# Optimization experiments

Measured on AMD Instinct MI355X. Metric: run time of the kernel, lower is better.

## Reference

```python
import jax, jax.numpy as jnp
import numpy as np

NUM_EMBEDDINGS = 512
EMBEDDING_DIM = 64
COMMITMENT_COST = 0.25


def setup_inputs() -> dict:
    key = jax.random.key(0)
    k1, k2 = jax.random.split(key)
    x = jax.random.normal(k1, (32, 64, 64, 64), dtype=jnp.float32)  # [B, C=D, H, W]
    # torch init: uniform(-1/K, 1/K)
    w = jax.random.uniform(k2, (NUM_EMBEDDINGS, EMBEDDING_DIM), dtype=jnp.float32,
                           minval=-1.0 / NUM_EMBEDDINGS, maxval=1.0 / NUM_EMBEDDINGS)
    return {"x": x, "w": w}


def reference(x, w):
    # [B, C, H, W] -> [B, H, W, C]
    xt = jnp.transpose(x, (0, 2, 3, 1))
    flat = xt.reshape(-1, EMBEDDING_DIM)  # [N, D]
    # squared L2 distances to each codebook vector: [N, K]
    distances = (jnp.sum(flat * flat, axis=1, keepdims=True)
                 + jnp.sum(w * w, axis=1)
                 - 2.0 * flat @ w.T)
    idx = jnp.argmin(distances, axis=1)  # [N]
    encodings = jax.nn.one_hot(idx, NUM_EMBEDDINGS, dtype=x.dtype)  # [N, K]
    quantized = w[idx].reshape(xt.shape)  # gather == one_hot @ w
    e_latent_loss = jnp.mean((jax.lax.stop_gradient(quantized) - xt) ** 2)
    q_latent_loss = jnp.mean((quantized - jax.lax.stop_gradient(xt)) ** 2)
    quant_loss = q_latent_loss + COMMITMENT_COST * e_latent_loss
    # straight-through estimator
    quantized_st = xt + jax.lax.stop_gradient(quantized - xt)
    quantized_out = jnp.transpose(quantized_st, (0, 3, 1, 2))  # back to [B, C, H, W]
    avg_probs = jnp.mean(encodings, axis=0)
    perplexity = jnp.exp(-jnp.sum(avg_probs * jnp.log(avg_probs + 1e-10)))
    return quantized_out, quant_loss, encodings, perplexity
```

## Files before the change

### kernel.cpp

```cpp
#include <hip/hip_runtime.h>
#include <math.h>

#define TB        256
#define POSB      64
#define GROUPS    4
#define KPG       128
#define NPOS      131072
#define KCODES    512
#define DIM       64
#define HW        4096
#define LOSS_OFF  8388608ull
#define ENC_OFF   8388609ull
#define PERP_OFF  75497473ull

__device__ __forceinline__ float tree8(float r0, float r1, float r2, float r3,
                                       float r4, float r5, float r6, float r7) {
    return __fadd_rn(__fadd_rn(__fadd_rn(r0, r1), __fadd_rn(r2, r3)),
                     __fadd_rn(__fadd_rn(r4, r5), __fadd_rn(r6, r7)));
}

extern "C" __global__ __launch_bounds__(512)
void vq_prep(const float* __restrict__ w, float* __restrict__ ww,
             int* __restrict__ counts, float* __restrict__ lossAcc)
{
    const int k = threadIdx.x;
    const float* wk = w + k * DIM;
    float r[8];
    #pragma unroll
    for (int i = 0; i < 8; ++i) {
        #pragma unroll
        for (int j = 0; j < 8; ++j) {
            float v = wk[i * 8 + j];
            float pp = __fmul_rn(v, v);
            r[j] = (i == 0) ? pp : __fadd_rn(r[j], pp);
        }
    }
    ww[k] = tree8(r[0], r[1], r[2], r[3], r[4], r[5], r[6], r[7]);
    counts[k] = 0;
    if (k == 0) *lossAcc = 0.0f;
}

extern "C" __global__ __launch_bounds__(TB)
__attribute__((amdgpu_waves_per_eu(2, 4)))
void vq_main(const float* __restrict__ x, const float* __restrict__ w,
             const float* __restrict__ ww, float* __restrict__ out,
             int* __restrict__ counts, float* __restrict__ lossAcc)
{
    __shared__ float cdist[GROUPS][POSB];
    __shared__ int   ckidx[GROUPS][POSB];
    __shared__ int   hcount[KCODES];

    const int tid = threadIdx.x;
    const int l   = tid & 63;
    const int g   = __builtin_amdgcn_readfirstlane(tid >> 6);
    const int n   = blockIdx.x * POSB + l;
    const int b   = n >> 12;
    const int hw  = n & 4095;

    hcount[tid]      = 0;
    hcount[tid + TB] = 0;

    const float* xp = x + ((size_t)b * DIM) * HW + hw;
    float x2[DIM];
    float r[8];
    #pragma unroll
    for (int i = 0; i < 8; ++i) {
        #pragma unroll
        for (int j = 0; j < 8; ++j) {
            const int d = i * 8 + j;
            float v = xp[(size_t)d * HW];
            x2[d] = v + v;
            float pp = __fmul_rn(v, v);
            r[j] = (i == 0) ? pp : __fadd_rn(r[j], pp);
        }
    }
    const float A = tree8(r[0], r[1], r[2], r[3], r[4], r[5], r[6], r[7]);

    float best  = INFINITY;
    int   bestk = 0;
    const size_t T0 = ENC_OFF + (size_t)blockIdx.x * (POSB * KCODES);
    float4* zs4 = reinterpret_cast<float4*>(out + T0 + 3);
    const float4 zero4 = make_float4(0.0f, 0.0f, 0.0f, 0.0f);

    for (int kk = 0; kk < KPG; ++kk) {
        const int k = g * KPG + kk;
        const float* wk = w + (size_t)k * DIM;
        float s[8];
        #pragma unroll
        for (int i = 0; i < 8; ++i) {
            #pragma unroll
            for (int j = 0; j < 8; ++j) {
                const int d = i * 8 + j;
                if (i == 0) s[j] = __fmul_rn(x2[d], wk[d]);
                else        s[j] = __fmaf_rn(x2[d], wk[d], s[j]);
            }
        }
        float dot  = tree8(s[0], s[1], s[2], s[3], s[4], s[5], s[6], s[7]);
        float t    = __fadd_rn(A, ww[k]);
        float dist = __fadd_rn(t, -dot);
        if (dist < best) { best = dist; bestk = k; }

        if ((kk & 3) == 0) {
            const int m = (kk >> 2) * TB + tid;
            if (m < 8191) zs4[m] = zero4;
        }
    }
    cdist[g][l] = best;
    ckidx[g][l] = bestk;

    if (tid < 3)  out[T0 + tid]   = 0.0f;
    if (tid == 3) out[T0 + 32767] = 0.0f;

    __syncthreads();

    float fb = cdist[0][l];
    int   fk = ckidx[0][l];
    #pragma unroll
    for (int gg = 1; gg < GROUPS; ++gg) {
        float dg = cdist[gg][l];
        int   kg = ckidx[gg][l];
        if (dg < fb) { fb = dg; fk = kg; }
    }

    if (g == 0) {
        out[ENC_OFF + (size_t)n * KCODES + fk] = 1.0f;
        atomicAdd(&hcount[fk], 1);

        const float4* wrow = reinterpret_cast<const float4*>(w + (size_t)fk * DIM);
        float* qo = out + ((size_t)b * DIM) * HW + hw;
        float sse = 0.0f;
        #pragma unroll
        for (int c = 0; c < 16; ++c) {
            float4 q = wrow[c];
            qo[(size_t)(4 * c + 0) * HW] = q.x;
            qo[(size_t)(4 * c + 1) * HW] = q.y;
            qo[(size_t)(4 * c + 2) * HW] = q.z;
            qo[(size_t)(4 * c + 3) * HW] = q.w;
            float e0 = q.x - 0.5f * x2[4 * c + 0]; sse = __fmaf_rn(e0, e0, sse);
            float e1 = q.y - 0.5f * x2[4 * c + 1]; sse = __fmaf_rn(e1, e1, sse);
            float e2 = q.z - 0.5f * x2[4 * c + 2]; sse = __fmaf_rn(e2, e2, sse);
            float e3 = q.w - 0.5f * x2[4 * c + 3]; sse = __fmaf_rn(e3, e3, sse);
        }
        #pragma unroll
        for (int off = 32; off > 0; off >>= 1) sse += __shfl_down(sse, off);
        if (l == 0) atomicAdd(lossAcc, sse);
    }

    __syncthreads();

    {
        int c0 = hcount[tid];       if (c0) atomicAdd(&counts[tid], c0);
        int c1 = hcount[tid + TB];  if (c1) atomicAdd(&counts[tid + TB], c1);
    }
}

extern "C" __global__ __launch_bounds__(512)
void vq_finalize(const int* __restrict__ counts, const float* __restrict__ lossAcc,
                 float* __restrict__ out)
{
    __shared__ double sred[KCODES];
    const int t = threadIdx.x;
    double p = (double)counts[t] * (1.0 / (double)NPOS);
    sred[t] = -p * log(p + 1e-10);
    __syncthreads();
    for (int s = KCODES / 2; s > 0; s >>= 1) {
        if (t < s) sred[t] += sred[t + s];
        __syncthreads();
    }
    if (t == 0) {
        out[PERP_OFF] = (float)exp(sred[0]);
        out[LOSS_OFF] = 1.25f * (lossAcc[0] / 8388608.0f);
    }
}

extern "C" void kernel_launch(void* const* d_in, const int* in_sizes, int n_in,
                              void* d_out, int out_size, void* d_ws, size_t ws_size,
                              hipStream_t stream)
{
    const float* x = (const float*)d_in[0];
    const float* w = (const float*)d_in[1];
    float* out = (float*)d_out;

    float* ww      = (float*)d_ws;
    int*   counts  = (int*)((char*)d_ws + 2048);
    float* lossAcc = (float*)((char*)d_ws + 4096);

    vq_prep<<<1, 512, 0, stream>>>(w, ww, counts, lossAcc);
    vq_main<<<NPOS / POSB, TB, 0, stream>>>(x, w, ww, out, counts, lossAcc);
    vq_finalize<<<1, 512, 0, stream>>>(counts, lossAcc, out);
}
```

Before: 447.1 us.

## Process two positions per thread to reuse codebook loads across positions

Each thread now handles two spatial positions (128 per block), so every codebook weight load feeds two FMAs, halving the weight-load traffic per distance computed. The grid shrinks by half, and the epilogue is split across two wavefronts, one for each position set. The per-thread register footprint roughly doubles (two 64-float x vectors), and waves_per_eu is pinned to 2 to allow that, which lowers occupancy.

```diff
diff --git a/kernel.cpp b/kernel.cpp
--- a/kernel.cpp
+++ b/kernel.cpp
@@ -2,7 +2,7 @@
 #include <math.h>
 
 #define TB        256
-#define POSB      64
+#define POSB      128
 #define GROUPS    4
 #define KPG       128
 #define NPOS      131072
@@ -12,6 +12,8 @@
 #define LOSS_OFF  8388608ull
 #define ENC_OFF   8388609ull
 #define PERP_OFF  75497473ull
+#define TILE_DW   (POSB * KCODES)
+#define NF4       ((TILE_DW - 4) / 4)
 
 __device__ __forceinline__ float tree8(float r0, float r1, float r2, float r3,
                                        float r4, float r5, float r6, float r7) {
@@ -40,8 +42,40 @@
     if (k == 0) *lossAcc = 0.0f;
 }
 
+#define EPILOGUE(X2, P)  do {                                                   \
+    const int p_ = (P);                                                         \
+    float fb = cdist[0][p_];                                                    \
+    int   fk = ckidx[0][p_];                                                    \
+    _Pragma("unroll")                                                           \
+    for (int gg = 1; gg < GROUPS; ++gg) {                                       \
+        float dg = cdist[gg][p_];                                               \
+        int   kg = ckidx[gg][p_];                                               \
+        if (dg < fb) { fb = dg; fk = kg; }                                      \
+    }                                                                           \
+    out[ENC_OFF + (size_t)(blockIdx.x * POSB + p_) * KCODES + fk] = 1.0f;       \
+    atomicAdd(&hcount[fk], 1);                                                  \
+    const float4* wrow = reinterpret_cast<const float4*>(w + (size_t)fk * DIM); \
+    float* qo = out + ((size_t)b * DIM) * HW + (hwb + p_);                      \
+    float sse = 0.0f;                                                           \
+    _Pragma("unroll")                                                           \
+    for (int c = 0; c < 16; ++c) {                                              \
+        float4 q = wrow[c];                                                     \
+        qo[(size_t)(4 * c + 0) * HW] = q.x;                                     \
+        qo[(size_t)(4 * c + 1) * HW] = q.y;                                     \
+        qo[(size_t)(4 * c + 2) * HW] = q.z;                                     \
+        qo[(size_t)(4 * c + 3) * HW] = q.w;                                     \
+        float e0 = q.x - 0.5f * X2[4 * c + 0]; sse = __fmaf_rn(e0, e0, sse);    \
+        float e1 = q.y - 0.5f * X2[4 * c + 1]; sse = __fmaf_rn(e1, e1, sse);    \
+        float e2 = q.z - 0.5f * X2[4 * c + 2]; sse = __fmaf_rn(e2, e2, sse);    \
+        float e3 = q.w - 0.5f * X2[4 * c + 3]; sse = __fmaf_rn(e3, e3, sse);    \
+    }                                                                           \
+    _Pragma("unroll")                                                           \
+    for (int off = 32; off > 0; off >>= 1) sse += __shfl_down(sse, off);        \
+    if (l == 0) atomicAdd(lossAcc, sse);                                        \
+} while (0)
+
 extern "C" __global__ __launch_bounds__(TB)
-__attribute__((amdgpu_waves_per_eu(2, 4)))
+__attribute__((amdgpu_waves_per_eu(2, 2)))
 void vq_main(const float* __restrict__ x, const float* __restrict__ w,
              const float* __restrict__ ww, float* __restrict__ out,
              int* __restrict__ counts, float* __restrict__ lossAcc)
@@ -53,98 +87,88 @@
     const int tid = threadIdx.x;
     const int l   = tid & 63;
     const int g   = __builtin_amdgcn_readfirstlane(tid >> 6);
-    const int n   = blockIdx.x * POSB + l;
-    const int b   = n >> 12;
-    const int hw  = n & 4095;
+    const int hwb = (blockIdx.x * POSB) & 4095;
+    const int b   = (blockIdx.x * POSB) >> 12;
 
     hcount[tid]      = 0;
     hcount[tid + TB] = 0;
 
-    const float* xp = x + ((size_t)b * DIM) * HW + hw;
-    float x2[DIM];
-    float r[8];
-    #pragma unroll
-    for (int i = 0; i < 8; ++i) {
-        #pragma unroll
-        for (int j = 0; j < 8; ++j) {
-            const int d = i * 8 + j;
-            float v = xp[(size_t)d * HW];
-            x2[d] = v + v;
-            float pp = __fmul_rn(v, v);
-            r[j] = (i == 0) ? pp : __fadd_rn(r[j], pp);
-        }
-    }
-    const float A = tree8(r[0], r[1], r[2], r[3], r[4], r[5], r[6], r[7]);
-
-    float best  = INFINITY;
-    int   bestk = 0;
-    const size_t T0 = ENC_OFF + (size_t)blockIdx.x * (POSB * KCODES);
-    float4* zs4 = reinterpret_cast<float4*>(out + T0 + 3);
-    const float4 zero4 = make_float4(0.0f, 0.0f, 0.0f, 0.0f);
-
-    for (int kk = 0; kk < KPG; ++kk) {
-        const int k = g * KPG + kk;
-        const float* wk = w + (size_t)k * DIM;
-        float s[8];
+    const float* xp = x + ((size_t)b * DIM) * HW + (hwb + l);
+    float x2a[DIM], x2b[DIM];
+    float A0, A1;
+    {
+        float ra[8], rb[8];
         #pragma unroll
         for (int i = 0; i < 8; ++i) {
             #pragma unroll
             for (int j = 0; j < 8; ++j) {
                 const int d = i * 8 + j;
-                if (i == 0) s[j] = __fmul_rn(x2[d], wk[d]);
-                else        s[j] = __fmaf_rn(x2[d], wk[d], s[j]);
+                float va = xp[(size_t)d * HW];
+                float vb = xp[(size_t)d * HW + 64];
+                x2a[d] = va + va;
+                x2b[d] = vb + vb;
+                float pa = __fmul_rn(va, va);
+                float pb = __fmul_rn(vb, vb);
+                ra[j] = (i == 0) ? pa : __fadd_rn(ra[j], pa);
+                rb[j] = (i == 0) ? pb : __fadd_rn(rb[j], pb);
             }
         }
-        float dot  = tree8(s[0], s[1], s[2], s[3], s[4], s[5], s[6], s[7]);
-        float t    = __fadd_rn(A, ww[k]);
-        float dist = __fadd_rn(t, -dot);
-        if (dist < best) { best = dist; bestk = k; }
-
-        if ((kk & 3) == 0) {
-            const int m = (kk >> 2) * TB + tid;
-            if (m < 8191) zs4[m] = zero4;
-        }
-    }
-    cdist[g][l] = best;
-    ckidx[g][l] = bestk;
-
-    if (tid < 3)  out[T0 + tid]   = 0.0f;
-    if (tid == 3) out[T0 + 32767] = 0.0f;
+        A0 = tree8(ra[0], ra[1], ra[2], ra[3], ra[4], ra[5], ra[6], ra[7]);
+        A1 = tree8(rb[0], rb[1], rb[2], rb[3], rb[4], rb[5], rb[6], rb[7]);
+    }
+
+    float best0 = INFINITY, best1 = INFINITY;
+    int   bk0 = 0, bk1 = 0;
+    const size_t T0 = ENC_OFF + (size_t)blockIdx.x * TILE_DW;
+    float4* zs4 = reinterpret_cast<float4*>(out + T0 + 3);
+    const float4 zero4 = make_float4(0.0f, 0.0f, 0.0f, 0.0f);
+
+    for (int kk = 0; kk < KPG; ++kk) {
+        const int k = g * KPG + kk;
+        const float* wk = w + (size_t)k * DIM;
+        float s0[8], s1[8];
+        #pragma unroll
+        for (int i = 0; i < 8; ++i) {
+            #pragma unroll
+            for (int j = 0; j < 8; ++j) {
+                const int d = i * 8 + j;
+                float wv = wk[d];
+                if (i == 0) {
+                    s0[j] = __fmul_rn(x2a[d], wv);
+                    s1[j] = __fmul_rn(x2b[d], wv);
+                } else {
+                    s0[j] = __fmaf_rn(x2a[d], wv, s0[j]);
+                    s1[j] = __fmaf_rn(x2b[d], wv, s1[j]);
+                }
+            }
+        }
+        float dot0 = tree8(s0[0], s0[1], s0[2], s0[3], s0[4], s0[5], s0[6], s0[7]);
+        float dot1 = tree8(s1[0], s1[1], s1[2], s1[3], s1[4], s1[5], s1[6], s1[7]);
+        float wwk  = ww[k];
+        float t0s  = __fadd_rn(A0, wwk);
+        float t1s  = __fadd_rn(A1, wwk);
+        float d0   = __fadd_rn(t0s, -dot0);
+        float d1   = __fadd_rn(t1s, -dot1);
+        if (d0 < best0) { best0 = d0; bk0 = k; }
+        if (d1 < best1) { best1 = d1; bk1 = k; }
+
+        if ((kk & 1) == 0) {
+            const int m = (kk >> 1) * TB + tid;
+            if (m < NF4) zs4[m] = zero4;
+        }
+    }
+    cdist[g][l]      = best0;
+    ckidx[g][l]      = bk0;
+    cdist[g][l + 64] = best1;
+    ckidx[g][l + 64] = bk1;
+
+    if (tid < 3)  out[T0 + tid] = 0.0f;
+    if (tid == 3) out[T0 + (TILE_DW - 1)] = 0.0f;
 
     __syncthreads();
 
-    float fb = cdist[0][l];
-    int   fk = ckidx[0][l];
-    #pragma unroll
-    for (int gg = 1; gg < GROUPS; ++gg) {
-        float dg = cdist[gg][l];
-        int   kg = ckidx[gg][l];
-        if (dg < fb) { fb = dg; fk = kg; }
-    }
-
-    if (g == 0) {
-        out[ENC_OFF + (size_t)n * KCODES + fk] = 1.0f;
-        atomicAdd(&hcount[fk], 1);
-
-        const float4* wrow = reinterpret_cast<const float4*>(w + (size_t)fk * DIM);
-        float* qo = out + ((size_t)b * DIM) * HW + hw;
-        float sse = 0.0f;
-        #pragma unroll
-        for (int c = 0; c < 16; ++c) {
-            float4 q = wrow[c];
-            qo[(size_t)(4 * c + 0) * HW] = q.x;
-            qo[(size_t)(4 * c + 1) * HW] = q.y;
-            qo[(size_t)(4 * c + 2) * HW] = q.z;
-            qo[(size_t)(4 * c + 3) * HW] = q.w;
-            float e0 = q.x - 0.5f * x2[4 * c + 0]; sse = __fmaf_rn(e0, e0, sse);
-            float e1 = q.y - 0.5f * x2[4 * c + 1]; sse = __fmaf_rn(e1, e1, sse);
-            float e2 = q.z - 0.5f * x2[4 * c + 2]; sse = __fmaf_rn(e2, e2, sse);
-            float e3 = q.w - 0.5f * x2[4 * c + 3]; sse = __fmaf_rn(e3, e3, sse);
-        }
-        #pragma unroll
-        for (int off = 32; off > 0; off >>= 1) sse += __shfl_down(sse, off);
-        if (l == 0) atomicAdd(lossAcc, sse);
-    }
+    if (g == 0)      { EPILOGUE(x2a, l); }
+    else if (g == 1) { EPILOGUE(x2b, l + 64); }
 
     __syncthreads();
 
```

After: 433.2 us. -3.1%, faster.

## Assign one position per thread and stage codebook through LDS in phases

Applied to the files above, without the earlier changes.

Each thread now owns one of 256 positions and scans all 512 codes itself, which removes the 4-way code-group split and its LDS argmin merge. Codebook rows are copied into shared memory in three phases of up to 240 rows, along with the precomputed row norms, so the inner loop reads LDS broadcasts instead of scalar or global loads. Zeroing of the one-hot tile is spread across the code loop as before. The trade-offs are 4x fewer blocks (512) with waves_per_eu pinned to 2, extra barriers per phase, and about 62KB of LDS per block, which limits occupancy. The inner loop is also no longer unrolled.

```diff
diff --git a/kernel.cpp b/kernel.cpp
--- a/kernel.cpp
+++ b/kernel.cpp
@@ -2,9 +2,7 @@
 #include <math.h>
 
 #define TB        256
-#define POSB      64
-#define GROUPS    4
-#define KPG       128
+#define POSB      256
 #define NPOS      131072
 #define KCODES    512
 #define DIM       64
@@ -12,6 +10,9 @@
 #define LOSS_OFF  8388608ull
 #define ENC_OFF   8388609ull
 #define PERP_OFF  75497473ull
+#define TILE_DW   (POSB * KCODES)
+#define NF4       ((TILE_DW - 4) / 4)
+#define ROWS_PP   240
 
 __device__ __forceinline__ float tree8(float r0, float r1, float r2, float r3,
                                        float r4, float r5, float r6, float r7) {
@@ -41,19 +42,18 @@
 }
 
 extern "C" __global__ __launch_bounds__(TB)
-__attribute__((amdgpu_waves_per_eu(2, 4)))
+__attribute__((amdgpu_waves_per_eu(2, 2)))
 void vq_main(const float* __restrict__ x, const float* __restrict__ w,
              const float* __restrict__ ww, float* __restrict__ out,
              int* __restrict__ counts, float* __restrict__ lossAcc)
 {
-    __shared__ float cdist[GROUPS][POSB];
-    __shared__ int   ckidx[GROUPS][POSB];
+    __shared__ __align__(16) float wlds[ROWS_PP * DIM];
+    __shared__ float wwlds[KCODES];
     __shared__ int   hcount[KCODES];
 
     const int tid = threadIdx.x;
     const int l   = tid & 63;
-    const int g   = __builtin_amdgcn_readfirstlane(tid >> 6);
-    const int n   = blockIdx.x * POSB + l;
+    const int n   = blockIdx.x * POSB + tid;
     const int b   = n >> 12;
     const int hw  = n & 4095;
 
@@ -62,89 +62,97 @@
 
     const float* xp = x + ((size_t)b * DIM) * HW + hw;
     float x2[DIM];
-    float r[8];
-    #pragma unroll
-    for (int i = 0; i < 8; ++i) {
-        #pragma unroll
-        for (int j = 0; j < 8; ++j) {
-            const int d = i * 8 + j;
-            float v = xp[(size_t)d * HW];
-            x2[d] = v + v;
-            float pp = __fmul_rn(v, v);
-            r[j] = (i == 0) ? pp : __fadd_rn(r[j], pp);
-        }
-    }
-    const float A = tree8(r[0], r[1], r[2], r[3], r[4], r[5], r[6], r[7]);
-
-    float best  = INFINITY;
-    int   bestk = 0;
-    const size_t T0 = ENC_OFF + (size_t)blockIdx.x * (POSB * KCODES);
-    float4* zs4 = reinterpret_cast<float4*>(out + T0 + 3);
-    const float4 zero4 = make_float4(0.0f, 0.0f, 0.0f, 0.0f);
-
-    for (int kk = 0; kk < KPG; ++kk) {
-        const int k = g * KPG + kk;
-        const float* wk = w + (size_t)k * DIM;
-        float s[8];
+    float A;
+    {
+        float r[8];
         #pragma unroll
         for (int i = 0; i < 8; ++i) {
             #pragma unroll
             for (int j = 0; j < 8; ++j) {
                 const int d = i * 8 + j;
-                if (i == 0) s[j] = __fmul_rn(x2[d], wk[d]);
-                else        s[j] = __fmaf_rn(x2[d], wk[d], s[j]);
+                float v = xp[(size_t)d * HW];
+                x2[d] = v + v;
+                float pp = __fmul_rn(v, v);
+                r[j] = (i == 0) ? pp : __fadd_rn(r[j], pp);
             }
         }
-        float dot  = tree8(s[0], s[1], s[2], s[3], s[4], s[5], s[6], s[7]);
-        float t    = __fadd_rn(A, ww[k]);
-        float dist = __fadd_rn(t, -dot);
-        if (dist < best) { best = dist; bestk = k; }
-
-        if ((kk & 3) == 0) {
-            const int m = (kk >> 2) * TB + tid;
-            if (m < 8191) zs4[m] = zero4;
-        }
-    }
-    cdist[g][l] = best;
-    ckidx[g][l] = bestk;
-
-    if (tid < 3)  out[T0 + tid]   = 0.0f;
-    if (tid == 3) out[T0 + 32767] = 0.0f;
-
-    __syncthreads();
-
-    float fb = cdist[0][l];
-    int   fk = ckidx[0][l];
-    #pragma unroll
-    for (int gg = 1; gg < GROUPS; ++gg) {
-        float dg = cdist[gg][l];
-        int   kg = ckidx[gg][l];
-        if (dg < fb) { fb = dg; fk = kg; }
+        A = tree8(r[0], r[1], r[2], r[3], r[4], r[5], r[6], r[7]);
     }
 
-    if (g == 0) {
-        out[ENC_OFF + (size_t)n * KCODES + fk] = 1.0f;
-        atomicAdd(&hcount[fk], 1);
+    const size_t T0 = ENC_OFF + (size_t)blockIdx.x * TILE_DW;
+    float4* zs4 = reinterpret_cast<float4*>(out + T0 + 3);
+    const float4 zero4 = make_float4(0.0f, 0.0f, 0.0f, 0.0f);
+    if (tid < 3)  out[T0 + tid] = 0.0f;
+    if (tid == 3) out[T0 + (TILE_DW - 1)] = 0.0f;
 
-        const float4* wrow = reinterpret_cast<const float4*>(w + (size_t)fk * DIM);
-        float* qo = out + ((size_t)b * DIM) * HW + hw;
-        float sse = 0.0f;
-        #pragma unroll
-        for (int c = 0; c < 16; ++c) {
-            float4 q = wrow[c];
-            qo[(size_t)(4 * c + 0) * HW] = q.x;
-            qo[(size_t)(4 * c + 1) * HW] = q.y;
-            qo[(size_t)(4 * c + 2) * HW] = q.z;
-            qo[(size_t)(4 * c + 3) * HW] = q.w;
-            float e0 = q.x - 0.5f * x2[4 * c + 0]; sse = __fmaf_rn(e0, e0, sse);
-            float e1 = q.y - 0.5f * x2[4 * c + 1]; sse = __fmaf_rn(e1, e1, sse);
-            float e2 = q.z - 0.5f * x2[4 * c + 2]; sse = __fmaf_rn(e2, e2, sse);
-            float e3 = q.w - 0.5f * x2[4 * c + 3]; sse = __fmaf_rn(e3, e3, sse);
+    float best  = INFINITY;
+    int   bestk = 0;
+
+    const float4* w4  = reinterpret_cast<const float4*>(w);
+    float4*       wl4 = reinterpret_cast<float4*>(wlds);
+
+    #pragma unroll 1
+    for (int p = 0; p < 3; ++p) {
+        const int k0 = (p == 0) ? 0 : ((p == 1) ? ROWS_PP : 2 * ROWS_PP);
+        const int k1 = (p == 2) ? KCODES : (k0 + ROWS_PP);
+
+        const int nf = (k1 - k0) * (DIM / 4);
+        for (int f = tid; f < nf; f += TB)
+            wl4[f] = w4[k0 * (DIM / 4) + f];
+        if (p == 0) {
+            wwlds[tid]      = ww[tid];
+            wwlds[tid + TB] = ww[tid + TB];
         }
-        #pragma unroll
-        for (int off = 32; off > 0; off >>= 1) sse += __shfl_down(sse, off);
-        if (l == 0) atomicAdd(lossAcc, sse);
+        __syncthreads();
+
+        #pragma unroll 1
+        for (int k = k0; k < k1; ++k) {
+            const float* row = wlds + (k - k0) * DIM;
+            float s[8];
+            #pragma unroll
+            for (int i = 0; i < 8; ++i) {
+                #pragma unroll
+                for (int j = 0; j < 8; ++j) {
+                    const int d = i * 8 + j;
+                    float wv = row[d];
+                    if (i == 0) s[j] = __fmul_rn(x2[d], wv);
+                    else        s[j] = __fmaf_rn(x2[d], wv, s[j]);
+                }
+            }
+            float dot  = tree8(s[0], s[1], s[2], s[3], s[4], s[5], s[6], s[7]);
+            float t    = __fadd_rn(A, wwlds[k]);
+            float dist = __fadd_rn(t, -dot);
+            if (dist < best) { best = dist; bestk = k; }
+
+            if ((k & 3) == 0) {
+                const int m = (k >> 2) * TB + tid;
+                if (m < NF4) zs4[m] = zero4;
+            }
+        }
+        __syncthreads();
     }
+
+    out[ENC_OFF + (size_t)n * KCODES + bestk] = 1.0f;
+    atomicAdd(&hcount[bestk], 1);
+
+    const float4* wrow = reinterpret_cast<const float4*>(w + (size_t)bestk * DIM);
+    float* qo = out + ((size_t)b * DIM) * HW + hw;
+    float sse = 0.0f;
+    #pragma unroll
+    for (int c = 0; c < 16; ++c) {
+        float4 q = wrow[c];
+        qo[(size_t)(4 * c + 0) * HW] = q.x;
+        qo[(size_t)(4 * c + 1) * HW] = q.y;
+        qo[(size_t)(4 * c + 2) * HW] = q.z;
+        qo[(size_t)(4 * c + 3) * HW] = q.w;
+        float e0 = q.x - 0.5f * x2[4 * c + 0]; sse = __fmaf_rn(e0, e0, sse);
+        float e1 = q.y - 0.5f * x2[4 * c + 1]; sse = __fmaf_rn(e1, e1, sse);
+        float e2 = q.z - 0.5f * x2[4 * c + 2]; sse = __fmaf_rn(e2, e2, sse);
+        float e3 = q.w - 0.5f * x2[4 * c + 3]; sse = __fmaf_rn(e3, e3, sse);
+    }
+    #pragma unroll
+    for (int off = 32; off > 0; off >>= 1) sse += __shfl_down(sse, off);
+    if (l == 0) atomicAdd(lossAcc, sse);
 
     __syncthreads();
 
```

Measured after the change: 531.8 us. 18.9% more time.
